# Kernel optimization log

Hardware: AMD Instinct MI355X
Metric: run time of the kernel (lower is better)

Reference implementation:

```python
import jax, jax.numpy as jnp
import numpy as np

EPS = 1e-6


def _make_coord_3d(D, H, W, dtype):
    # torch make_coord_3d(flatten=False).permute(3,0,1,2): channels stacked as (x, y, z)
    lz = jnp.linspace(-1.0, 1.0, D, dtype=dtype)
    ly = jnp.linspace(-1.0, 1.0, H, dtype=dtype)
    lx = jnp.linspace(-1.0, 1.0, W, dtype=dtype)
    cz, cy, cx = jnp.meshgrid(lz, ly, lx, indexing='ij')
    return jnp.stack([cx, cy, cz], axis=0)  # [3, D, H, W]


def _trilinear_border(vol, gd, gh, gw):
    # vol: [C, D, H, W]; gd/gh/gw: [Q] normalized coords for the D/H/W axes.
    # Matches torch grid_sample(mode='bilinear', align_corners=False, padding_mode='border').
    C, D, H, W = vol.shape
    z = (gd + 1.0) * (D * 0.5) - 0.5
    y = (gh + 1.0) * (H * 0.5) - 0.5
    x = (gw + 1.0) * (W * 0.5) - 0.5
    z0 = jnp.floor(z); y0 = jnp.floor(y); x0 = jnp.floor(x)
    wz = (z - z0)[None]; wy = (y - y0)[None]; wx = (x - x0)[None]  # [1, Q]
    z0i = jnp.clip(z0.astype(jnp.int32), 0, D - 1); z1i = jnp.clip(z0.astype(jnp.int32) + 1, 0, D - 1)
    y0i = jnp.clip(y0.astype(jnp.int32), 0, H - 1); y1i = jnp.clip(y0.astype(jnp.int32) + 1, 0, H - 1)
    x0i = jnp.clip(x0.astype(jnp.int32), 0, W - 1); x1i = jnp.clip(x0.astype(jnp.int32) + 1, 0, W - 1)
    g = lambda zi, yi, xi: vol[:, zi, yi, xi]  # gather -> [C, Q]
    return (g(z0i, y0i, x0i) * (1 - wz) * (1 - wy) * (1 - wx)
            + g(z0i, y0i, x1i) * (1 - wz) * (1 - wy) * wx
            + g(z0i, y1i, x0i) * (1 - wz) * wy * (1 - wx)
            + g(z0i, y1i, x1i) * (1 - wz) * wy * wx
            + g(z1i, y0i, x0i) * wz * (1 - wy) * (1 - wx)
            + g(z1i, y0i, x1i) * wz * (1 - wy) * wx
            + g(z1i, y1i, x0i) * wz * wy * (1 - wx)
            + g(z1i, y1i, x1i) * wz * wy * wx)


def _forward(inp, coord, cell, W0, b0, W1, b1, W2, b2, W3, b3):
    feat = inp  # identity encoder: inp is the latent feature grid
    B, C, D, H, W = feat.shape
    rx = 2.0 / D / 2.0; ry = 2.0 / H / 2.0; rz = 2.0 / W / 2.0
    sizes = jnp.array([D, H, W], dtype=feat.dtype)
    feat_coord = _make_coord_3d(D, H, W, feat.dtype)  # [3, D, H, W]
    sample_b = jax.vmap(_trilinear_border, in_axes=(0, 0, 0, 0))
    sample_c = jax.vmap(_trilinear_border, in_axes=(None, 0, 0, 0))

    rel_cell = cell * sizes  # [B, Q, 3]
    cell_vol = jnp.abs(cell[..., 0] * cell[..., 1] * cell[..., 2])
    scale_sq = jnp.clip(8.0 / (cell_vol + 1e-8), 1.0, 64.0)[..., None]  # [B, Q, 1]

    def mlp(x):
        h = jax.nn.relu(x @ W0 + b0)
        h = jax.nn.relu(h @ W1 + b1)
        h = jax.nn.relu(h @ W2 + b2)
        return h @ W3 + b3

    preds, areas = [], []
    for vx in (-1, 1):
        for vy in (-1, 1):
            for vz in (-1, 1):
                shift = jnp.array([vx * rx + EPS, vy * ry + EPS, vz * rz + EPS], dtype=coord.dtype)
                c = jnp.clip(coord + shift, -1.0 + 1e-6, 1.0 - 1e-6)
                gd, gh, gw = c[..., 0], c[..., 1], c[..., 2]
                q_feat = sample_b(feat, gd, gh, gw).transpose(0, 2, 1)        # [B, Q, C]
                q_coord = sample_c(feat_coord, gd, gh, gw).transpose(0, 2, 1)  # [B, Q, 3]
                rel_coord = (coord - q_coord) * sizes
                x = jnp.concatenate([q_feat, rel_coord, rel_cell, scale_sq], axis=-1)
                preds.append(mlp(x))  # [B, Q, 1]
                areas.append(jnp.abs(rel_coord[..., 0] * rel_coord[..., 1] * rel_coord[..., 2]) + 1e-9)
    tot_area = jnp.stack(areas).sum(axis=0)
    areas = areas[::-1]  # local-ensemble diagonal-swap of areas
    ret = sum(p * (a / tot_area)[..., None] for p, a in zip(preds, areas))
    return ret


def setup_inputs() -> dict:
    key = jax.random.key(0)
    ks = jax.random.split(key, 8)
    B, C, D, Q, HID = 1, 64, 32, 131072, 256
    in_dim = C + 3 + 3 + 1  # 71
    w = lambda k, shape, fan_in: jax.random.normal(k, shape, jnp.float32) * (1.0 / np.sqrt(fan_in))
    inp = jax.random.normal(ks[0], (B, C, D, D, D), jnp.float32)
    coord = jax.random.uniform(ks[1], (B, Q, 3), jnp.float32, -1.0, 1.0)
    cell = jnp.full((B, Q, 3), 2.0 / 64.0, jnp.float32)  # uniform cell size of a 64^3 query grid
    return {
        'inp': inp, 'coord': coord, 'cell': cell,
        'W0': w(ks[2], (in_dim, HID), in_dim), 'b0': jnp.zeros((HID,), jnp.float32),
        'W1': w(ks[3], (HID, HID), HID), 'b1': jnp.zeros((HID,), jnp.float32),
        'W2': w(ks[4], (HID, HID), HID), 'b2': jnp.zeros((HID,), jnp.float32),
        'W3': w(ks[5], (HID, 1), HID), 'b3': jnp.zeros((1,), jnp.float32),
    }


def reference(inp, coord, cell, W0, b0, W1, b1, W2, b2, W3, b3):
    return _forward(inp, coord, cell, W0, b0, W1, b1, W2, b2, W3, b3)
```

## Files before the change

kernel.cpp:

```cpp
#include <hip/hip_runtime.h>

typedef __attribute__((ext_vector_type(8))) short s16x8;
typedef __attribute__((ext_vector_type(4))) float f32x4;

__device__ __forceinline__ unsigned short f2bf(float x) {
  unsigned u = __float_as_uint(x);
  u = (u + 0x7fffu + ((u >> 16) & 1u)) >> 16;
  return (unsigned short)u;
}
__device__ __forceinline__ float bflo(unsigned v) { return __uint_as_float(v << 16); }
__device__ __forceinline__ float bfhi(unsigned v) { return __uint_as_float(v & 0xffff0000u); }

#define FEAT_OFF 0
#define W0F_OFF  2097152
#define W1F_OFF  (W0F_OFF + 24576)
#define W2F_OFF  (W1F_OFF + 65536)
#define WS_TOTAL (W2F_OFF + 65536)

__global__ void liif_prep(const float* __restrict__ inp,
                          const float* __restrict__ W0,
                          const float* __restrict__ W1,
                          const float* __restrict__ W2,
                          unsigned short* __restrict__ ws) {
  int tid = blockIdx.x * 256 + threadIdx.x;
  if (tid < 2097152) {
    int pos = tid >> 6, c = tid & 63;
    ws[FEAT_OFF + tid] = f2bf(inp[c * 32768 + pos]);
  } else if (tid < W1F_OFF) {
    int e = tid - W0F_OFF;
    int j = e & 7, L = (e >> 3) & 63, nt = (e >> 9) & 15, c = e >> 13;
    int k = c * 32 + (L >> 4) * 8 + j, n = nt * 16 + (L & 15);
    ws[tid] = (k < 71) ? f2bf(W0[k * 256 + n]) : (unsigned short)0;
  } else if (tid < W2F_OFF) {
    int e = tid - W1F_OFF;
    int j = e & 7, L = (e >> 3) & 63, nt = (e >> 9) & 15, c = e >> 13;
    int k = c * 32 + (L >> 4) * 8 + j, n = nt * 16 + (L & 15);
    ws[tid] = f2bf(W1[k * 256 + n]);
  } else if (tid < WS_TOTAL) {
    int e = tid - W2F_OFF;
    int j = e & 7, L = (e >> 3) & 63, nt = (e >> 9) & 15, c = e >> 13;
    int k = c * 32 + (L >> 4) * 8 + j, n = nt * 16 + (L & 15);
    ws[tid] = f2bf(W2[k * 256 + n]);
  }
}

template<int KC>
__device__ __forceinline__ void run_layer(const unsigned short* __restrict__ Wf,
                                          const float* __restrict__ bias,
                                          const unsigned short* A, int astride,
                                          unsigned short* H,
                                          int wave, int quad, int l16, int lane) {
  f32x4 acc[4][4];
#pragma unroll
  for (int i = 0; i < 4; ++i)
#pragma unroll
    for (int j = 0; j < 4; ++j) acc[i][j] = (f32x4){0.f, 0.f, 0.f, 0.f};

#pragma unroll
  for (int c = 0; c < KC; ++c) {
    s16x8 a[4];
#pragma unroll
    for (int rt = 0; rt < 4; ++rt)
      a[rt] = *(const s16x8*)(A + (rt * 16 + l16) * astride + c * 32 + quad * 8);
#pragma unroll
    for (int ntl = 0; ntl < 4; ++ntl) {
      int nt = wave * 4 + ntl;
      s16x8 b = *(const s16x8*)(Wf + (((c * 16 + nt) * 64 + lane) << 3));
#pragma unroll
      for (int rt = 0; rt < 4; ++rt)
        acc[rt][ntl] = __builtin_amdgcn_mfma_f32_16x16x32_bf16(a[rt], b, acc[rt][ntl], 0, 0, 0);
    }
  }
  __syncthreads();
#pragma unroll
  for (int ntl = 0; ntl < 4; ++ntl) {
    int col = (wave * 4 + ntl) * 16 + l16;
    float bv = bias[col];
#pragma unroll
    for (int rt = 0; rt < 4; ++rt) {
#pragma unroll
      for (int i = 0; i < 4; ++i) {
        int r = rt * 16 + quad * 4 + i;
        float h = fmaxf(acc[rt][ntl][i] + bv, 0.0f);
        H[r * 264 + col] = f2bf(h);
      }
    }
  }
  __syncthreads();
}

__global__ __launch_bounds__(256, 3)
void liif_main(const float* __restrict__ coord,
               const float* __restrict__ cell,
               const float* __restrict__ b0,
               const float* __restrict__ b1,
               const float* __restrict__ b2,
               const float* __restrict__ W3,
               const float* __restrict__ b3,
               const unsigned short* __restrict__ ws,
               float* __restrict__ out) {
  __shared__ __align__(16) unsigned short sm_x[64 * 104];
  __shared__ __align__(16) unsigned short sm_h[64 * 264];
  __shared__ float sm_area[64];
  __shared__ float sm_pred[64];

  const unsigned short* feat = ws + FEAT_OFF;
  const int tid = threadIdx.x;
  const int lane = tid & 63;
  const int wave = tid >> 6;
  const int quad = lane >> 4;
  const int l16 = lane & 15;

  {
    const int row = tid >> 2, p = tid & 3;
    const int ql = row >> 3, s = row & 7;
    const int q = blockIdx.x * 8 + ql;
    const float c0r = coord[q * 3 + 0], c1r = coord[q * 3 + 1], c2r = coord[q * 3 + 2];
    const float R = 0.03125f;
    const float sh0 = ((s & 4) ? R : -R) + 1e-6f;
    const float sh1 = ((s & 2) ? R : -R) + 1e-6f;
    const float sh2 = ((s & 1) ? R : -R) + 1e-6f;
    const float LO = -1.0f + 1e-6f, HI = 1.0f - 1e-6f;
    float c0 = fminf(fmaxf(c0r + sh0, LO), HI);
    float c1 = fminf(fmaxf(c1r + sh1, LO), HI);
    float c2 = fminf(fmaxf(c2r + sh2, LO), HI);
    float z = (c0 + 1.0f) * 16.0f - 0.5f;
    float y = (c1 + 1.0f) * 16.0f - 0.5f;
    float x = (c2 + 1.0f) * 16.0f - 0.5f;
    float zf = floorf(z), yf = floorf(y), xf = floorf(x);
    float wz = z - zf, wy = y - yf, wx = x - xf;
    int z0 = min(max((int)zf, 0), 31), z1 = min(max((int)zf + 1, 0), 31);
    int y0 = min(max((int)yf, 0), 31), y1 = min(max((int)yf + 1, 0), 31);
    int x0 = min(max((int)xf, 0), 31), x1 = min(max((int)xf + 1, 0), 31);
    float wz0 = 1.0f - wz, wy0 = 1.0f - wy, wx0 = 1.0f - wx;

    float w[8] = { wz0 * wy0 * wx0, wz0 * wy0 * wx, wz0 * wy * wx0, wz0 * wy * wx,
                   wz  * wy0 * wx0, wz  * wy0 * wx, wz  * wy * wx0, wz  * wy * wx };
    int idx[8] = { (z0 * 32 + y0) * 32 + x0, (z0 * 32 + y0) * 32 + x1,
                   (z0 * 32 + y1) * 32 + x0, (z0 * 32 + y1) * 32 + x1,
                   (z1 * 32 + y0) * 32 + x0, (z1 * 32 + y0) * 32 + x1,
                   (z1 * 32 + y1) * 32 + x0, (z1 * 32 + y1) * 32 + x1 };

    float acc[16];
#pragma unroll
    for (int i = 0; i < 16; ++i) acc[i] = 0.0f;
#pragma unroll
    for (int corner = 0; corner < 8; ++corner) {
      const uint4* cp = (const uint4*)(feat + idx[corner] * 64 + p * 16);
      uint4 v0 = cp[0], v1 = cp[1];
      float wc = w[corner];
      unsigned vv[8] = { v0.x, v0.y, v0.z, v0.w, v1.x, v1.y, v1.z, v1.w };
#pragma unroll
      for (int d = 0; d < 8; ++d) {
        acc[2 * d]     += wc * bflo(vv[d]);
        acc[2 * d + 1] += wc * bfhi(vv[d]);
      }
    }
    unsigned pw[8];
#pragma unroll
    for (int d = 0; d < 8; ++d)
      pw[d] = (unsigned)f2bf(acc[2 * d]) | ((unsigned)f2bf(acc[2 * d + 1]) << 16);
    uint4* dst = (uint4*)(&sm_x[row * 104 + p * 16]);
    dst[0] = make_uint4(pw[0], pw[1], pw[2], pw[3]);
    dst[1] = make_uint4(pw[4], pw[5], pw[6], pw[7]);

    if (p == 0) {
      const float step = 2.0f / 31.0f;
      float qc0 = wx0 * (-1.0f + step * x0) + wx * (-1.0f + step * x1);
      float qc1 = wy0 * (-1.0f + step * y0) + wy * (-1.0f + step * y1);
      float qc2 = wz0 * (-1.0f + step * z0) + wz * (-1.0f + step * z1);
      float rel0 = (c0r - qc0) * 32.0f;
      float rel1 = (c1r - qc1) * 32.0f;
      float rel2 = (c2r - qc2) * 32.0f;
      sm_area[row] = fabsf(rel0 * rel1 * rel2) + 1e-9f;
      float cl0 = cell[q * 3 + 0], cl1 = cell[q * 3 + 1], cl2 = cell[q * 3 + 2];
      float ssq = fminf(fmaxf(8.0f / (fabsf(cl0 * cl1 * cl2) + 1e-8f), 1.0f), 64.0f);
      unsigned tw0 = (unsigned)f2bf(rel0) | ((unsigned)f2bf(rel1) << 16);
      unsigned tw1 = (unsigned)f2bf(rel2) | ((unsigned)f2bf(cl0 * 32.0f) << 16);
      unsigned tw2 = (unsigned)f2bf(cl1 * 32.0f) | ((unsigned)f2bf(cl2 * 32.0f) << 16);
      unsigned tw3 = (unsigned)f2bf(ssq);
      uint4* d2 = (uint4*)(&sm_x[row * 104 + 64]);
      d2[0] = make_uint4(tw0, tw1, tw2, tw3);
      d2[1] = make_uint4(0, 0, 0, 0);
      d2[2] = make_uint4(0, 0, 0, 0);
      d2[3] = make_uint4(0, 0, 0, 0);
    }
  }
  __syncthreads();

  run_layer<3>(ws + W0F_OFF, b0, sm_x, 104, sm_h, wave, quad, l16, lane);
  run_layer<8>(ws + W1F_OFF, b1, sm_h, 264, sm_h, wave, quad, l16, lane);
  run_layer<8>(ws + W2F_OFF, b2, sm_h, 264, sm_h, wave, quad, l16, lane);

  {
    const int row = tid >> 2, p = tid & 3;
    const unsigned short* hp = sm_h + row * 264 + p * 64;
    float sum = 0.0f;
#pragma unroll
    for (int kk = 0; kk < 8; ++kk) {
      const uint4 v = *(const uint4*)(hp + kk * 8);
      const float* w = W3 + p * 64 + kk * 8;
      unsigned vv[4] = { v.x, v.y, v.z, v.w };
#pragma unroll
      for (int d = 0; d < 4; ++d) {
        sum += w[2 * d]     * bflo(vv[d]);
        sum += w[2 * d + 1] * bfhi(vv[d]);
      }
    }
    sum += __shfl_xor(sum, 1);
    sum += __shfl_xor(sum, 2);
    if (p == 0) sm_pred[row] = sum + b3[0];
  }
  __syncthreads();

  if (tid < 8) {
    const int ql = tid;
    float tot = 0.0f, ret = 0.0f;
#pragma unroll
    for (int s = 0; s < 8; ++s) tot += sm_area[ql * 8 + s];
#pragma unroll
    for (int s = 0; s < 8; ++s) ret += sm_pred[ql * 8 + s] * sm_area[ql * 8 + (7 - s)];
    out[blockIdx.x * 8 + ql] = ret / tot;
  }
}

extern "C" void kernel_launch(void* const* d_in, const int* in_sizes, int n_in,
                              void* d_out, int out_size, void* d_ws, size_t ws_size,
                              hipStream_t stream) {
  const float* inp   = (const float*)d_in[0];
  const float* coord = (const float*)d_in[1];
  const float* cell  = (const float*)d_in[2];
  const float* W0    = (const float*)d_in[3];
  const float* b0    = (const float*)d_in[4];
  const float* W1    = (const float*)d_in[5];
  const float* b1    = (const float*)d_in[6];
  const float* W2    = (const float*)d_in[7];
  const float* b2    = (const float*)d_in[8];
  const float* W3    = (const float*)d_in[9];
  const float* b3    = (const float*)d_in[10];
  unsigned short* ws = (unsigned short*)d_ws;
  float* out = (float*)d_out;

  const int Q = in_sizes[1] / 3;
  hipLaunchKernelGGL(liif_prep, dim3((WS_TOTAL + 255) / 256), dim3(256), 0, stream,
                     inp, W0, W1, W2, ws);
  hipLaunchKernelGGL(liif_main, dim3(Q / 8), dim3(256), 0, stream,
                     coord, cell, b0, b1, b2, W3, b3, ws, out);
}
```

Before: 494.7 us.

## Permute hidden columns for packed bf16 stores, alias LDS buffers, raise occupancy

The layer epilogue now writes four adjacent bf16 values per 8-byte LDS store, using the hardware packed bf16 convert. To keep the math unchanged, the hidden-unit columns are stored in a permuted order, and the K rows of W1, W2 and W3 are permuted to match in the prep kernel. The input staging buffer now aliases the hidden buffer, which cuts LDS use, and launch bounds rise to 4 blocks per CU. The risks are register pressure under the tighter launch bound and subtle indexing errors in the permutation.

```diff
diff --git a/kernel.cpp b/kernel.cpp
--- a/kernel.cpp
+++ b/kernel.cpp
@@ -8,6 +8,11 @@
   u = (u + 0x7fffu + ((u >> 16) & 1u)) >> 16;
   return (unsigned short)u;
 }
+__device__ __forceinline__ unsigned cvt_pk_bf16(float a, float b) {
+  unsigned r;
+  asm("v_cvt_pk_bf16_f32 %0, %1, %2" : "=v"(r) : "v"(a), "v"(b));
+  return r;
+}
 __device__ __forceinline__ float bflo(unsigned v) { return __uint_as_float(v << 16); }
 __device__ __forceinline__ float bfhi(unsigned v) { return __uint_as_float(v & 0xffff0000u); }
 
@@ -15,12 +20,18 @@
 #define W0F_OFF  2097152
 #define W1F_OFF  (W0F_OFF + 24576)
 #define W2F_OFF  (W1F_OFF + 65536)
-#define WS_TOTAL (W2F_OFF + 65536)
+#define W3P_OFF  (W2F_OFF + 65536)
+#define WS_TOTAL (W3P_OFF + 512)
+
+__device__ __forceinline__ int col_log(int kp) {
+  return (kp & 0xC0) | ((kp & 3) << 4) | ((kp >> 2) & 15);
+}
 
 __global__ void liif_prep(const float* __restrict__ inp,
                           const float* __restrict__ W0,
                           const float* __restrict__ W1,
                           const float* __restrict__ W2,
+                          const float* __restrict__ W3,
                           unsigned short* __restrict__ ws) {
   int tid = blockIdx.x * 256 + threadIdx.x;
   if (tid < 2097152) {
@@ -34,13 +45,17 @@
   } else if (tid < W2F_OFF) {
     int e = tid - W1F_OFF;
     int j = e & 7, L = (e >> 3) & 63, nt = (e >> 9) & 15, c = e >> 13;
-    int k = c * 32 + (L >> 4) * 8 + j, n = nt * 16 + (L & 15);
-    ws[tid] = f2bf(W1[k * 256 + n]);
-  } else if (tid < WS_TOTAL) {
+    int kp = c * 32 + (L >> 4) * 8 + j, n = nt * 16 + (L & 15);
+    ws[tid] = f2bf(W1[col_log(kp) * 256 + n]);
+  } else if (tid < W3P_OFF) {
     int e = tid - W2F_OFF;
     int j = e & 7, L = (e >> 3) & 63, nt = (e >> 9) & 15, c = e >> 13;
-    int k = c * 32 + (L >> 4) * 8 + j, n = nt * 16 + (L & 15);
-    ws[tid] = f2bf(W2[k * 256 + n]);
+    int kp = c * 32 + (L >> 4) * 8 + j, n = nt * 16 + (L & 15);
+    ws[tid] = f2bf(W2[col_log(kp) * 256 + n]);
+  } else if (tid < W3P_OFF + 256) {
+    int e = tid - W3P_OFF;
+    float* w3p = (float*)(ws + W3P_OFF);
+    w3p[e] = W3[col_log(e)];
   }
 }
 
@@ -72,37 +87,41 @@
     }
   }
   __syncthreads();
-#pragma unroll
-  for (int ntl = 0; ntl < 4; ++ntl) {
-    int col = (wave * 4 + ntl) * 16 + l16;
-    float bv = bias[col];
-#pragma unroll
-    for (int rt = 0; rt < 4; ++rt) {
-#pragma unroll
-      for (int i = 0; i < 4; ++i) {
-        int r = rt * 16 + quad * 4 + i;
-        float h = fmaxf(acc[rt][ntl][i] + bv, 0.0f);
-        H[r * 264 + col] = f2bf(h);
-      }
-    }
-  }
-  __syncthreads();
-}
-
-__global__ __launch_bounds__(256, 3)
+
+  float bv[4];
+#pragma unroll
+  for (int ntl = 0; ntl < 4; ++ntl) bv[ntl] = bias[(wave * 4 + ntl) * 16 + l16];
+
+  const int cbase = wave * 64 + l16 * 4;
+#pragma unroll
+  for (int rt = 0; rt < 4; ++rt) {
+#pragma unroll
+    for (int i = 0; i < 4; ++i) {
+      float v0 = fmaxf(acc[rt][0][i] + bv[0], 0.0f);
+      float v1 = fmaxf(acc[rt][1][i] + bv[1], 0.0f);
+      float v2 = fmaxf(acc[rt][2][i] + bv[2], 0.0f);
+      float v3 = fmaxf(acc[rt][3][i] + bv[3], 0.0f);
+      int r = rt * 16 + quad * 4 + i;
+      uint2 pw = make_uint2(cvt_pk_bf16(v0, v1), cvt_pk_bf16(v2, v3));
+      *(uint2*)(H + r * 264 + cbase) = pw;
+    }
+  }
+  __syncthreads();
+}
+
+__global__ __launch_bounds__(256, 4)
 void liif_main(const float* __restrict__ coord,
                const float* __restrict__ cell,
                const float* __restrict__ b0,
                const float* __restrict__ b1,
                const float* __restrict__ b2,
-               const float* __restrict__ W3,
                const float* __restrict__ b3,
                const unsigned short* __restrict__ ws,
                float* __restrict__ out) {
-  __shared__ __align__(16) unsigned short sm_x[64 * 104];
   __shared__ __align__(16) unsigned short sm_h[64 * 264];
   __shared__ float sm_area[64];
   __shared__ float sm_pred[64];
+  unsigned short* sm_x = sm_h;
 
   const unsigned short* feat = ws + FEAT_OFF;
   const int tid = threadIdx.x;
@@ -159,7 +178,7 @@
     unsigned pw[8];
 #pragma unroll
     for (int d = 0; d < 8; ++d)
-      pw[d] = (unsigned)f2bf(acc[2 * d]) | ((unsigned)f2bf(acc[2 * d + 1]) << 16);
+      pw[d] = cvt_pk_bf16(acc[2 * d], acc[2 * d + 1]);
     uint4* dst = (uint4*)(&sm_x[row * 104 + p * 16]);
     dst[0] = make_uint4(pw[0], pw[1], pw[2], pw[3]);
     dst[1] = make_uint4(pw[4], pw[5], pw[6], pw[7]);
@@ -175,10 +194,10 @@
       sm_area[row] = fabsf(rel0 * rel1 * rel2) + 1e-9f;
       float cl0 = cell[q * 3 + 0], cl1 = cell[q * 3 + 1], cl2 = cell[q * 3 + 2];
       float ssq = fminf(fmaxf(8.0f / (fabsf(cl0 * cl1 * cl2) + 1e-8f), 1.0f), 64.0f);
-      unsigned tw0 = (unsigned)f2bf(rel0) | ((unsigned)f2bf(rel1) << 16);
-      unsigned tw1 = (unsigned)f2bf(rel2) | ((unsigned)f2bf(cl0 * 32.0f) << 16);
-      unsigned tw2 = (unsigned)f2bf(cl1 * 32.0f) | ((unsigned)f2bf(cl2 * 32.0f) << 16);
-      unsigned tw3 = (unsigned)f2bf(ssq);
+      unsigned tw0 = cvt_pk_bf16(rel0, rel1);
+      unsigned tw1 = cvt_pk_bf16(rel2, cl0 * 32.0f);
+      unsigned tw2 = cvt_pk_bf16(cl1 * 32.0f, cl2 * 32.0f);
+      unsigned tw3 = cvt_pk_bf16(ssq, 0.0f);
       uint4* d2 = (uint4*)(&sm_x[row * 104 + 64]);
       d2[0] = make_uint4(tw0, tw1, tw2, tw3);
       d2[1] = make_uint4(0, 0, 0, 0);
@@ -195,17 +214,17 @@
   {
     const int row = tid >> 2, p = tid & 3;
     const unsigned short* hp = sm_h + row * 264 + p * 64;
+    const float* W3p = (const float*)(ws + W3P_OFF);
     float sum = 0.0f;
 #pragma unroll
     for (int kk = 0; kk < 8; ++kk) {
       const uint4 v = *(const uint4*)(hp + kk * 8);
-      const float* w = W3 + p * 64 + kk * 8;
-      unsigned vv[4] = { v.x, v.y, v.z, v.w };
-#pragma unroll
-      for (int d = 0; d < 4; ++d) {
-        sum += w[2 * d]     * bflo(vv[d]);
-        sum += w[2 * d + 1] * bfhi(vv[d]);
-      }
+      const float4 wa = *(const float4*)(W3p + p * 64 + kk * 8);
+      const float4 wb = *(const float4*)(W3p + p * 64 + kk * 8 + 4);
+      sum += wa.x * bflo(v.x) + wa.y * bfhi(v.x);
+      sum += wa.z * bflo(v.y) + wa.w * bfhi(v.y);
+      sum += wb.x * bflo(v.z) + wb.y * bfhi(v.z);
+      sum += wb.z * bflo(v.w) + wb.w * bfhi(v.w);
     }
     sum += __shfl_xor(sum, 1);
     sum += __shfl_xor(sum, 2);
@@ -243,7 +262,7 @@
 
   const int Q = in_sizes[1] / 3;
   hipLaunchKernelGGL(liif_prep, dim3((WS_TOTAL + 255) / 256), dim3(256), 0, stream,
-                     inp, W0, W1, W2, ws);
+                     inp, W0, W1, W2, W3, ws);
   hipLaunchKernelGGL(liif_main, dim3(Q / 8), dim3(256), 0, stream,
-                     coord, cell, b0, b1, b2, W3, b3, ws, out);
-}
+                     coord, cell, b0, b1, b2, b3, ws, out);
+}
```

Result: faster. 461.9 us (-6.6%).
